# Performance work log

Measured on AMD Instinct MI355X. Metric: run time of the kernel, lower is better.

## Reference

```python
import jax, jax.numpy as jnp
import numpy as np

B, H, S, D = 4, 8, 2048, 64

def setup_inputs() -> dict:
    key = jax.random.key(0)
    k1, k2 = jax.random.split(key)
    q = jax.random.normal(k1, (B, H, S, D), dtype=jnp.float32)
    kv = jax.random.normal(k2, (B, H, S, D), dtype=jnp.float32)
    mask = jnp.zeros((1, 1, S, S), dtype=jnp.float32)
    return {"q": q, "kv": kv, "mask": mask}

def reference(q, kv, mask):
    # score = q @ kv^T / sqrt(d_k) + mask ; softmax over last dim ; @ kv
    d_k = jnp.asarray(kv.shape[-1], dtype=q.dtype)
    score = jnp.einsum('bhqd,bhkd->bhqk', q, kv) / jnp.sqrt(d_k)
    score = score + mask
    attn = jax.nn.softmax(score, axis=-1)
    out = jnp.einsum('bhqk,bhkd->bhqd', attn, kv)
    return out
```

## Files before the change

kernel.cpp:

```cpp
#include <hip/hip_runtime.h>
#include <hip/hip_bf16.h>
#include <stdint.h>


typedef __bf16 bf16;
typedef __attribute__((ext_vector_type(8))) __bf16 bf16x8;
typedef __attribute__((ext_vector_type(4))) __bf16 bf16x4;
typedef __attribute__((ext_vector_type(4))) float floatx4;
typedef __attribute__((ext_vector_type(16))) float floatx16;
typedef __attribute__((ext_vector_type(4))) int int4v;
typedef __attribute__((ext_vector_type(2))) unsigned int uint2v;

#define SLEN 2048
#define DH   64
#define BR   64
#define BC   64
#define NKT  (SLEN / BC)
#define NQT  (SLEN / BR)
#define BH_N 32
#define LOG2E 1.44269504088896341f

#define IMGE_G 4096

#define AS1 __attribute__((address_space(1)))
#define AS3 __attribute__((address_space(3)))

static __device__ inline float fexp2(float x) {
    return __builtin_amdgcn_exp2f(x);
}

static_assert(BH_N == NQT, "prep kernel folds bh and qt onto one grid axis");

__global__ __launch_bounds__(256) void kv_prep(
    const float* __restrict__ kv, const float* __restrict__ mask,
    bf16* __restrict__ kvK, bf16* __restrict__ kvT, int* __restrict__ flags)
{
    __shared__ bf16 Tl[64 * 72];
    __shared__ int wany[4];
    const int kt = blockIdx.x, z = blockIdx.y;
    const int t = threadIdx.x;

    float acc = 0.f;
#pragma unroll
    for (int i = 0; i < 4; ++i) {
        int f = i * 256 + t;
        int row = f >> 4, c4 = (f & 15) * 4;
        const float4 v = *(const float4*)(mask + (size_t)(z * BR + row) * SLEN + kt * BC + c4);
        acc = fmaxf(acc, fmaxf(fmaxf(fabsf(v.x), fabsf(v.y)), fmaxf(fabsf(v.z), fabsf(v.w))));
    }
    unsigned long long any = __ballot(acc != 0.f);
    if ((t & 63) == 0) wany[t >> 6] = (any != 0ull) ? 1 : 0;

    const float* src = kv + ((size_t)z * SLEN + kt * BC) * DH;
#pragma unroll
    for (int i = 0; i < 4; ++i) {
        int f = i * 256 + t;
        int key = f >> 4, d4 = (f & 15) * 4;
        float4 v = *(const float4*)(src + (size_t)key * DH + d4);
        bf16x4 b; b[0] = (bf16)v.x; b[1] = (bf16)v.y; b[2] = (bf16)v.z; b[3] = (bf16)v.w;
        *(bf16x4*)&Tl[key * 72 + d4] = b;
    }
    __syncthreads();
    if (t == 0) flags[z * NKT + kt] = wany[0] | wany[1] | wany[2] | wany[3];

    bf16* outK = kvK + ((size_t)z * NKT + kt) * IMGE_G;
#pragma unroll
    for (int i = 0; i < 2; ++i) {
        int G = i * 256 + t;
        int u = G >> 8, ss = (G >> 6) & 3, ln = G & 63;
        int key = u * 32 + (ln & 31), d0 = 16 * ss + 8 * (ln >> 5);
        bf16x8 w = *(const bf16x8*)&Tl[key * 72 + d0];
        *(bf16x8*)(outK + (size_t)G * 8) = w;
    }
    bf16* outV = kvT + ((size_t)z * NKT + kt) * IMGE_G;
#pragma unroll
    for (int i = 0; i < 2; ++i) {
        int G = i * 256 + t;
        int dt = G >> 8, u = (G >> 7) & 1, ff = (G >> 6) & 1, ln = G & 63;
        int d = dt * 32 + (ln & 31), kb = u * 32 + 16 * ff + 8 * (ln >> 5);
        bf16x8 w;
#pragma unroll
        for (int j = 0; j < 8; ++j)
            w[j] = Tl[(kb + j) * 72 + d];
        *(bf16x8*)(outV + (size_t)G * 8) = w;
    }
}

__global__ __launch_bounds__(256) void attn_fwd20(
    const float* __restrict__ q, const float* __restrict__ mask,
    const int* __restrict__ flags,
    const bf16* __restrict__ kvK, const bf16* __restrict__ kvT,
    float* __restrict__ out)
{
    __shared__ __align__(16) float Obuf[2 * 2 * 4 * 64 * 4];
    __shared__ float Lbuf[2 * 64];

    const int bh = blockIdx.x;
    const int qt = blockIdx.y;
    const int q0 = qt * 64;
    const int t = threadIdx.x;
    const int w = t >> 6, lane = t & 63;
    const int qg = w & 1, kh = w >> 1;
    const int r5 = lane & 31, h = lane >> 5;

    const float qscale = 0.125f * LOG2E;
    bf16x8 qf[4];
    {
        const float* qrow = q + ((size_t)bh * SLEN + q0 + qg * 32 + r5) * DH;
#pragma unroll
        for (int s = 0; s < 4; ++s) {
            float4 f0 = *(const float4*)(qrow + 16 * s + 8 * h);
            float4 f1 = *(const float4*)(qrow + 16 * s + 8 * h + 4);
            bf16x8 a;
            a[0] = (bf16)(f0.x * qscale); a[1] = (bf16)(f0.y * qscale);
            a[2] = (bf16)(f0.z * qscale); a[3] = (bf16)(f0.w * qscale);
            a[4] = (bf16)(f1.x * qscale); a[5] = (bf16)(f1.y * qscale);
            a[6] = (bf16)(f1.z * qscale); a[7] = (bf16)(f1.w * qscale);
            qf[s] = a;
        }
    }

    unsigned fmask;
    {
        int ld = (lane < 32) ? flags[qt * NKT + lane] : 0;
        fmask = (unsigned)__ballot(ld != 0);
    }

    floatx16 o[2];
#pragma unroll
    for (int dt = 0; dt < 2; ++dt)
#pragma unroll
        for (int i = 0; i < 16; ++i) o[dt][i] = 0.f;
    float l_run = 0.f;

    const char* Kb = (const char*)(kvK + (size_t)bh * NKT * IMGE_G) + lane * 16;
    const char* Vb = (const char*)(kvT + (size_t)bh * NKT * IMGE_G) + lane * 16;

    bf16x8 ka0, ka1, ka2, ka3, va0, va1, va2, va3;
    bf16x8 kb0, kb1, kb2, kb3, vb0, vb1, vb2, vb3;

#define LOAD_SUB(K0,K1,K2,K3,V0,V1,V2,V3, j)                                  \
    {                                                                          \
        const int jj = (j) & 31;                                               \
        const char* Kt = Kb + (size_t)(kh * 16 + (jj >> 1)) * 8192 + (jj & 1) * 4096; \
        const char* Vt = Vb + (size_t)(kh * 16 + (jj >> 1)) * 8192 + (jj & 1) * 2048; \
        K0 = *(const bf16x8*)(Kt);                                             \
        K1 = *(const bf16x8*)(Kt + 1024);                                      \
        K2 = *(const bf16x8*)(Kt + 2048);                                      \
        K3 = *(const bf16x8*)(Kt + 3072);                                      \
        V0 = *(const bf16x8*)(Vt);                                             \
        V1 = *(const bf16x8*)(Vt + 1024);                                      \
        V2 = *(const bf16x8*)(Vt + 4096);                                      \
        V3 = *(const bf16x8*)(Vt + 4096 + 1024);                               \
    }

#define COMPUTE_SUB(K0,K1,K2,K3,V0,V1,V2,V3, j)                               \
    {                                                                          \
        const int jj = (j);                                                    \
        const int kt_ = kh * 16 + (jj >> 1);                                   \
        floatx16 s;                                                            \
        _Pragma("unroll")                                                      \
        for (int i = 0; i < 16; ++i) s[i] = 0.f;                               \
        s = __builtin_amdgcn_mfma_f32_32x32x16_bf16(K0, qf[0], s, 0, 0, 0);    \
        s = __builtin_amdgcn_mfma_f32_32x32x16_bf16(K1, qf[1], s, 0, 0, 0);    \
        s = __builtin_amdgcn_mfma_f32_32x32x16_bf16(K2, qf[2], s, 0, 0, 0);    \
        s = __builtin_amdgcn_mfma_f32_32x32x16_bf16(K3, qf[3], s, 0, 0, 0);    \
        if ((fmask >> kt_) & 1u) {                                             \
            const float* mrow = mask + (size_t)(q0 + qg * 32 + r5) * SLEN      \
                                + kt_ * 64 + (jj & 1) * 32 + 4 * h;            \
            _Pragma("unroll")                                                  \
            for (int g4 = 0; g4 < 4; ++g4) {                                   \
                float4 mv = *(const float4*)(mrow + 8 * g4);                   \
                s[4 * g4 + 0] += mv.x * LOG2E;                                 \
                s[4 * g4 + 1] += mv.y * LOG2E;                                 \
                s[4 * g4 + 2] += mv.z * LOG2E;                                 \
                s[4 * g4 + 3] += mv.w * LOG2E;                                 \
            }                                                                  \
        }                                                                      \
        _Pragma("unroll")                                                      \
        for (int i = 0; i < 16; ++i) s[i] = fexp2(s[i]);                       \
        l_run += ((s[0] + s[1]) + (s[2] + s[3]))                               \
               + ((s[4] + s[5]) + (s[6] + s[7]))                               \
               + ((s[8] + s[9]) + (s[10] + s[11]))                             \
               + ((s[12] + s[13]) + (s[14] + s[15]));                          \
        bf16x4 lA = { (bf16)s[0],  (bf16)s[1],  (bf16)s[2],  (bf16)s[3]  };    \
        bf16x4 hA = { (bf16)s[4],  (bf16)s[5],  (bf16)s[6],  (bf16)s[7]  };    \
        bf16x4 lB = { (bf16)s[8],  (bf16)s[9],  (bf16)s[10], (bf16)s[11] };    \
        bf16x4 hB = { (bf16)s[12], (bf16)s[13], (bf16)s[14], (bf16)s[15] };    \
        uint2v xA = __builtin_bit_cast(uint2v, lA);                            \
        uint2v yA = __builtin_bit_cast(uint2v, hA);                            \
        uint2v xB = __builtin_bit_cast(uint2v, lB);                            \
        uint2v yB = __builtin_bit_cast(uint2v, hB);                            \
        uint2v sA0 = __builtin_amdgcn_permlane32_swap(xA[0], yA[0], false, false); \
        uint2v sA1 = __builtin_amdgcn_permlane32_swap(xA[1], yA[1], false, false); \
        uint2v sB0 = __builtin_amdgcn_permlane32_swap(xB[0], yB[0], false, false); \
        uint2v sB1 = __builtin_amdgcn_permlane32_swap(xB[1], yB[1], false, false); \
        int4v pAi = { (int)sA0[0], (int)sA1[0], (int)sA0[1], (int)sA1[1] };    \
        int4v pBi = { (int)sB0[0], (int)sB1[0], (int)sB0[1], (int)sB1[1] };    \
        bf16x8 pfA = __builtin_bit_cast(bf16x8, pAi);                          \
        bf16x8 pfB = __builtin_bit_cast(bf16x8, pBi);                          \
        o[0] = __builtin_amdgcn_mfma_f32_32x32x16_bf16(V0, pfA, o[0], 0, 0, 0); \
        o[0] = __builtin_amdgcn_mfma_f32_32x32x16_bf16(V1, pfB, o[0], 0, 0, 0); \
        o[1] = __builtin_amdgcn_mfma_f32_32x32x16_bf16(V2, pfA, o[1], 0, 0, 0); \
        o[1] = __builtin_amdgcn_mfma_f32_32x32x16_bf16(V3, pfB, o[1], 0, 0, 0); \
    }

    LOAD_SUB(ka0, ka1, ka2, ka3, va0, va1, va2, va3, 0)

    for (int it = 0; it < 16; ++it) {
        const int j0 = 2 * it, j1 = 2 * it + 1;
        LOAD_SUB(kb0, kb1, kb2, kb3, vb0, vb1, vb2, vb3, j1)
        COMPUTE_SUB(ka0, ka1, ka2, ka3, va0, va1, va2, va3, j0)
        LOAD_SUB(ka0, ka1, ka2, ka3, va0, va1, va2, va3, j1 + 1)
        COMPUTE_SUB(kb0, kb1, kb2, kb3, vb0, vb1, vb2, vb3, j1)
    }
#undef LOAD_SUB
#undef COMPUTE_SUB

    __syncthreads();
    if (kh == 1) {
#pragma unroll
        for (int dt = 0; dt < 2; ++dt)
#pragma unroll
            for (int k = 0; k < 4; ++k) {
                float4 v;
                v.x = o[dt][4 * k + 0]; v.y = o[dt][4 * k + 1];
                v.z = o[dt][4 * k + 2]; v.w = o[dt][4 * k + 3];
                *(float4*)(Obuf + ((size_t)((qg * 2 + dt) * 4 + k) * 64 + lane) * 4) = v;
            }
        Lbuf[qg * 64 + lane] = l_run;
    }
    __syncthreads();
    if (kh == 0) {
        float lsum = l_run + Lbuf[qg * 64 + lane];
        float l = lsum + __shfl_xor(lsum, 32);
        float inv = 1.f / l;
        float* ob = out + ((size_t)bh * SLEN + q0 + qg * 32 + r5) * DH + 4 * h;
#pragma unroll
        for (int dt = 0; dt < 2; ++dt)
#pragma unroll
            for (int k = 0; k < 4; ++k) {
                float4 p = *(const float4*)(Obuf + ((size_t)((qg * 2 + dt) * 4 + k) * 64 + lane) * 4);
                float4 v;
                v.x = (o[dt][4 * k + 0] + p.x) * inv;
                v.y = (o[dt][4 * k + 1] + p.y) * inv;
                v.z = (o[dt][4 * k + 2] + p.z) * inv;
                v.w = (o[dt][4 * k + 3] + p.w) * inv;
                *(float4*)(ob + dt * 32 + 8 * k) = v;
            }
    }
}

#define LDT 72
__global__ __launch_bounds__(256) void attn_mask_flags(
    const float* __restrict__ mask, int* __restrict__ flags)
{
    const int kt = blockIdx.x, qt = blockIdx.y;
    const int t = threadIdx.x;
    float acc = 0.f;
#pragma unroll
    for (int i = 0; i < 4; ++i) {
        int f = i * 256 + t;
        int row = f >> 4, c4 = (f & 15) * 4;
        const float4 v = *(const float4*)(mask + (size_t)(qt * BR + row) * SLEN + kt * BC + c4);
        acc = fmaxf(acc, fmaxf(fmaxf(fabsf(v.x), fabsf(v.y)), fmaxf(fabsf(v.z), fabsf(v.w))));
    }
    unsigned long long any = __ballot(acc != 0.f);
    __shared__ int wany[4];
    if ((t & 63) == 0) wany[t >> 6] = (any != 0ull) ? 1 : 0;
    __syncthreads();
    if (t == 0) flags[qt * NKT + kt] = wany[0] | wany[1] | wany[2] | wany[3];
}

__global__ __launch_bounds__(256) void attn_fwd(
    const float* __restrict__ q, const float* __restrict__ kv,
    const float* __restrict__ mask, const int* __restrict__ flags,
    float* __restrict__ out)
{
    __shared__ __align__(16) bf16 Kl[BC * LDT];
    __shared__ __align__(16) bf16 Vt[DH * LDT];
    __shared__ __align__(16) bf16 Pl[BR * LDT];

    const int qt = blockIdx.x;
    const int bh = blockIdx.y;
    const int q0 = qt * BR;
    const int t = threadIdx.x;
    const int wave = t >> 6, lane = t & 63;
    const int ln16 = lane & 15, quad = lane >> 4;

    const float qscale = 0.125f * LOG2E;
    bf16x8 aq[2];
    {
        const float* qrow = q + ((size_t)bh * SLEN + q0 + wave * 16 + ln16) * DH;
#pragma unroll
        for (int kc = 0; kc < 2; ++kc) {
            float4 f0 = *(const float4*)(qrow + kc * 32 + quad * 8);
            float4 f1 = *(const float4*)(qrow + kc * 32 + quad * 8 + 4);
            bf16x8 a;
            a[0] = (bf16)(f0.x * qscale); a[1] = (bf16)(f0.y * qscale);
            a[2] = (bf16)(f0.z * qscale); a[3] = (bf16)(f0.w * qscale);
            a[4] = (bf16)(f1.x * qscale); a[5] = (bf16)(f1.y * qscale);
            a[6] = (bf16)(f1.z * qscale); a[7] = (bf16)(f1.w * qscale);
            aq[kc] = a;
        }
    }

    floatx4 o[4];
#pragma unroll
    for (int dt = 0; dt < 4; ++dt) o[dt] = (floatx4){0.f, 0.f, 0.f, 0.f};
    float m_run[4], l_run[4];
#pragma unroll
    for (int r = 0; r < 4; ++r) { m_run[r] = -3.0e38f; l_run[r] = 0.f; }

    const float* kvb = kv + (size_t)bh * SLEN * DH;

    for (int kt = 0; kt < NKT; ++kt) {
        float4 st[4];
        const float* kvt = kvb + (size_t)kt * BC * DH;
#pragma unroll
        for (int i = 0; i < 4; ++i) {
            int f = i * 256 + t;
            st[i] = *(const float4*)(kvt + (size_t)f * 4);
        }
        __syncthreads();
#pragma unroll
        for (int i = 0; i < 4; ++i) {
            int f = i * 256 + t;
            int key = f >> 4, d4 = (f & 15) * 4;
            bf16 b0 = (bf16)st[i].x, b1 = (bf16)st[i].y, b2 = (bf16)st[i].z, b3 = (bf16)st[i].w;
            *(bf16x4*)&Kl[key * LDT + d4] = (bf16x4){b0, b1, b2, b3};
            Vt[(d4 + 0) * LDT + key] = b0;
            Vt[(d4 + 1) * LDT + key] = b1;
            Vt[(d4 + 2) * LDT + key] = b2;
            Vt[(d4 + 3) * LDT + key] = b3;
        }
        __syncthreads();

        floatx4 s[4];
#pragma unroll
        for (int nt = 0; nt < 4; ++nt) {
            s[nt] = (floatx4){0.f, 0.f, 0.f, 0.f};
#pragma unroll
            for (int kc = 0; kc < 2; ++kc) {
                bf16x8 bk = *(const bf16x8*)&Kl[(ln16 + 16 * nt) * LDT + kc * 32 + quad * 8];
                s[nt] = __builtin_amdgcn_mfma_f32_16x16x32_bf16(aq[kc], bk, s[nt], 0, 0, 0);
            }
        }

        if (!flags || flags[qt * NKT + kt]) {
            const float* mrow = mask + (size_t)(q0 + quad * 4) * SLEN + kt * BC + ln16;
#pragma unroll
            for (int r = 0; r < 4; ++r)
#pragma unroll
                for (int nt = 0; nt < 4; ++nt)
                    s[nt][r] += mrow[(size_t)r * SLEN + nt * 16] * LOG2E;
        }

#pragma unroll
        for (int r = 0; r < 4; ++r) {
            float mx = fmaxf(fmaxf(s[0][r], s[1][r]), fmaxf(s[2][r], s[3][r]));
            mx = fmaxf(mx, __shfl_xor(mx, 1));
            mx = fmaxf(mx, __shfl_xor(mx, 2));
            mx = fmaxf(mx, __shfl_xor(mx, 4));
            mx = fmaxf(mx, __shfl_xor(mx, 8));
            float mnew = fmaxf(m_run[r], mx);
            float alpha = exp2f(m_run[r] - mnew);
            m_run[r] = mnew;
            float rs = 0.f;
#pragma unroll
            for (int nt = 0; nt < 4; ++nt) {
                float p = exp2f(s[nt][r] - mnew);
                s[nt][r] = p;
                rs += p;
            }
            rs += __shfl_xor(rs, 1);
            rs += __shfl_xor(rs, 2);
            rs += __shfl_xor(rs, 4);
            rs += __shfl_xor(rs, 8);
            l_run[r] = l_run[r] * alpha + rs;
#pragma unroll
            for (int dt = 0; dt < 4; ++dt) o[dt][r] *= alpha;
        }

#pragma unroll
        for (int nt = 0; nt < 4; ++nt)
#pragma unroll
            for (int r = 0; r < 4; ++r)
                Pl[(wave * 16 + quad * 4 + r) * LDT + ln16 + 16 * nt] = (bf16)s[nt][r];

#pragma unroll
        for (int kc2 = 0; kc2 < 2; ++kc2) {
            bf16x8 pfr = *(const bf16x8*)&Pl[(wave * 16 + ln16) * LDT + kc2 * 32 + quad * 8];
#pragma unroll
            for (int dt = 0; dt < 4; ++dt) {
                bf16x8 vfr = *(const bf16x8*)&Vt[(ln16 + 16 * dt) * LDT + kc2 * 32 + quad * 8];
                o[dt] = __builtin_amdgcn_mfma_f32_16x16x32_bf16(pfr, vfr, o[dt], 0, 0, 0);
            }
        }
    }

#pragma unroll
    for (int r = 0; r < 4; ++r) {
        float inv = 1.0f / l_run[r];
        int qrow = q0 + wave * 16 + quad * 4 + r;
        float* orow = out + ((size_t)bh * SLEN + qrow) * DH;
#pragma unroll
        for (int dt = 0; dt < 4; ++dt)
            orow[ln16 + 16 * dt] = o[dt][r] * inv;
    }
}

extern "C" void kernel_launch(void* const* d_in, const int* in_sizes, int n_in,
                              void* d_out, int out_size, void* d_ws, size_t ws_size,
                              hipStream_t stream)
{
    const float* q    = (const float*)d_in[0];
    const float* kv   = (const float*)d_in[1];
    const float* mask = (const float*)d_in[2];
    float* out = (float*)d_out;

    const size_t kvKoff = 4096;
    const size_t kvToff = kvKoff + (size_t)BH_N * NKT * IMGE_G * 2;
    const size_t need   = kvToff + (size_t)BH_N * NKT * IMGE_G * 2;

    if (ws_size >= need) {
        int*  flags = (int*)d_ws;
        bf16* kvK   = (bf16*)((char*)d_ws + kvKoff);
        bf16* kvT   = (bf16*)((char*)d_ws + kvToff);
        kv_prep<<<dim3(NKT, BH_N), 256, 0, stream>>>(kv, mask, kvK, kvT, flags);
        attn_fwd20<<<dim3(BH_N, SLEN / 64), 256, 0, stream>>>(q, mask, flags, kvK, kvT, out);
    } else {
        int* flags = nullptr;
        if (ws_size >= (size_t)NQT * NKT * sizeof(int)) {
            flags = (int*)d_ws;
            attn_mask_flags<<<dim3(NKT, NQT), 256, 0, stream>>>(mask, flags);
        }
        attn_fwd<<<dim3(NQT, BH_N), 256, 0, stream>>>(q, kv, mask, flags, out);
    }
}
```

Before: 139.4 us.

## Use 512-thread blocks over 128 query rows and software-pipeline QK with softmax/PV

Each block now covers 128 query rows with 8 waves (4 query groups by 2 key halves) instead of 64 rows with 4 waves, so blocks sharing a bh reuse the same K/V stream across more queries. The inner loop is restructured so the QK MFMAs for the next sub-tile are issued before the exp/PV work of the current one. V loads move into the finish step, so only K is double-buffered in registers. The aim is to overlap matrix work with exponentials and cut register pressure, at the risk of fewer blocks (512 instead of 1024) and exposed V load latency.

```diff
diff --git a/kernel.cpp b/kernel.cpp
--- a/kernel.cpp
+++ b/kernel.cpp
@@ -86,21 +86,21 @@
     }
 }
 
-__global__ __launch_bounds__(256) void attn_fwd20(
+__global__ __launch_bounds__(512) void attn_fwd25(
     const float* __restrict__ q, const float* __restrict__ mask,
     const int* __restrict__ flags,
     const bf16* __restrict__ kvK, const bf16* __restrict__ kvT,
     float* __restrict__ out)
 {
-    __shared__ __align__(16) float Obuf[2 * 2 * 4 * 64 * 4];
-    __shared__ float Lbuf[2 * 64];
+    __shared__ __align__(16) float Obuf[4 * 2 * 4 * 64 * 4];
+    __shared__ float Lbuf[4 * 64];
 
     const int bh = blockIdx.x;
     const int qt = blockIdx.y;
-    const int q0 = qt * 64;
+    const int q0 = qt * 128;
     const int t = threadIdx.x;
     const int w = t >> 6, lane = t & 63;
-    const int qg = w & 1, kh = w >> 1;
+    const int qg = w & 3, kh = w >> 2;
     const int r5 = lane & 31, h = lane >> 5;
 
     const float qscale = 0.125f * LOG2E;
@@ -120,114 +120,121 @@
         }
     }
 
+    const int fqt = qt * 2 + (qg >> 1);
     unsigned fmask;
     {
-        int ld = (lane < 32) ? flags[qt * NKT + lane] : 0;
+        int ld = (lane < 32) ? flags[fqt * NKT + lane] : 0;
         fmask = (unsigned)__ballot(ld != 0);
     }
 
-    floatx16 o[2];
-#pragma unroll
-    for (int dt = 0; dt < 2; ++dt)
-#pragma unroll
-        for (int i = 0; i < 16; ++i) o[dt][i] = 0.f;
+    floatx16 o0, o1;
+#pragma unroll
+    for (int i = 0; i < 16; ++i) { o0[i] = 0.f; o1[i] = 0.f; }
     float l_run = 0.f;
 
     const char* Kb = (const char*)(kvK + (size_t)bh * NKT * IMGE_G) + lane * 16;
     const char* Vb = (const char*)(kvT + (size_t)bh * NKT * IMGE_G) + lane * 16;
 
-    bf16x8 ka0, ka1, ka2, ka3, va0, va1, va2, va3;
-    bf16x8 kb0, kb1, kb2, kb3, vb0, vb1, vb2, vb3;
-
-#define LOAD_SUB(K0,K1,K2,K3,V0,V1,V2,V3, j)                                  \
+    bf16x8 kA0, kA1, kA2, kA3, kB0, kB1, kB2, kB3;
+    floatx16 sA, sB;
+
+#define LOADK(K0,K1,K2,K3, j)                                                  \
     {                                                                          \
-        const int jj = (j) & 31;                                               \
-        const char* Kt = Kb + (size_t)(kh * 16 + (jj >> 1)) * 8192 + (jj & 1) * 4096; \
-        const char* Vt = Vb + (size_t)(kh * 16 + (jj >> 1)) * 8192 + (jj & 1) * 2048; \
-        K0 = *(const bf16x8*)(Kt);                                             \
-        K1 = *(const bf16x8*)(Kt + 1024);                                      \
-        K2 = *(const bf16x8*)(Kt + 2048);                                      \
-        K3 = *(const bf16x8*)(Kt + 3072);                                      \
-        V0 = *(const bf16x8*)(Vt);                                             \
-        V1 = *(const bf16x8*)(Vt + 1024);                                      \
-        V2 = *(const bf16x8*)(Vt + 4096);                                      \
-        V3 = *(const bf16x8*)(Vt + 4096 + 1024);                               \
-    }
-
-#define COMPUTE_SUB(K0,K1,K2,K3,V0,V1,V2,V3, j)                               \
+        const char* Kt_ = Kb + (size_t)(kh * 16 + (((j) & 31) >> 1)) * 8192    \
+                          + ((j) & 1) * 4096;                                  \
+        K0 = *(const bf16x8*)(Kt_);                                            \
+        K1 = *(const bf16x8*)(Kt_ + 1024);                                     \
+        K2 = *(const bf16x8*)(Kt_ + 2048);                                     \
+        K3 = *(const bf16x8*)(Kt_ + 3072);                                     \
+    }
+
+#define QK(S, K0,K1,K2,K3)                                                     \
     {                                                                          \
-        const int jj = (j);                                                    \
-        const int kt_ = kh * 16 + (jj >> 1);                                   \
-        floatx16 s;                                                            \
         _Pragma("unroll")                                                      \
-        for (int i = 0; i < 16; ++i) s[i] = 0.f;                               \
-        s = __builtin_amdgcn_mfma_f32_32x32x16_bf16(K0, qf[0], s, 0, 0, 0);    \
-        s = __builtin_amdgcn_mfma_f32_32x32x16_bf16(K1, qf[1], s, 0, 0, 0);    \
-        s = __builtin_amdgcn_mfma_f32_32x32x16_bf16(K2, qf[2], s, 0, 0, 0);    \
-        s = __builtin_amdgcn_mfma_f32_32x32x16_bf16(K3, qf[3], s, 0, 0, 0);    \
+        for (int i = 0; i < 16; ++i) S[i] = 0.f;                               \
+        S = __builtin_amdgcn_mfma_f32_32x32x16_bf16(K0, qf[0], S, 0, 0, 0);    \
+        S = __builtin_amdgcn_mfma_f32_32x32x16_bf16(K1, qf[1], S, 0, 0, 0);    \
+        S = __builtin_amdgcn_mfma_f32_32x32x16_bf16(K2, qf[2], S, 0, 0, 0);    \
+        S = __builtin_amdgcn_mfma_f32_32x32x16_bf16(K3, qf[3], S, 0, 0, 0);    \
+    }
+
+#define FINISH(S, j)                                                           \
+    {                                                                          \
+        const int kt_ = kh * 16 + ((j) >> 1);                                  \
+        const char* Vt_ = Vb + (size_t)kt_ * 8192 + ((j) & 1) * 2048;          \
+        bf16x8 v00 = *(const bf16x8*)(Vt_);                                    \
+        bf16x8 v01 = *(const bf16x8*)(Vt_ + 1024);                             \
+        bf16x8 v10 = *(const bf16x8*)(Vt_ + 4096);                             \
+        bf16x8 v11 = *(const bf16x8*)(Vt_ + 4096 + 1024);                      \
         if ((fmask >> kt_) & 1u) {                                             \
             const float* mrow = mask + (size_t)(q0 + qg * 32 + r5) * SLEN      \
-                                + kt_ * 64 + (jj & 1) * 32 + 4 * h;            \
+                                + kt_ * 64 + ((j) & 1) * 32 + 4 * h;           \
             _Pragma("unroll")                                                  \
             for (int g4 = 0; g4 < 4; ++g4) {                                   \
                 float4 mv = *(const float4*)(mrow + 8 * g4);                   \
-                s[4 * g4 + 0] += mv.x * LOG2E;                                 \
-                s[4 * g4 + 1] += mv.y * LOG2E;                                 \
-                s[4 * g4 + 2] += mv.z * LOG2E;                                 \
-                s[4 * g4 + 3] += mv.w * LOG2E;                                 \
+                S[4 * g4 + 0] += mv.x * LOG2E;                                 \
+                S[4 * g4 + 1] += mv.y * LOG2E;                                 \
+                S[4 * g4 + 2] += mv.z * LOG2E;                                 \
+                S[4 * g4 + 3] += mv.w * LOG2E;                                 \
             }                                                                  \
         }                                                                      \
         _Pragma("unroll")                                                      \
-        for (int i = 0; i < 16; ++i) s[i] = fexp2(s[i]);                       \
-        l_run += ((s[0] + s[1]) + (s[2] + s[3]))                               \
-               + ((s[4] + s[5]) + (s[6] + s[7]))                               \
-               + ((s[8] + s[9]) + (s[10] + s[11]))                             \
-               + ((s[12] + s[13]) + (s[14] + s[15]));                          \
-        bf16x4 lA = { (bf16)s[0],  (bf16)s[1],  (bf16)s[2],  (bf16)s[3]  };    \
-        bf16x4 hA = { (bf16)s[4],  (bf16)s[5],  (bf16)s[6],  (bf16)s[7]  };    \
-        bf16x4 lB = { (bf16)s[8],  (bf16)s[9],  (bf16)s[10], (bf16)s[11] };    \
-        bf16x4 hB = { (bf16)s[12], (bf16)s[13], (bf16)s[14], (bf16)s[15] };    \
+        for (int i = 0; i < 16; ++i) S[i] = fexp2(S[i]);                       \
+        l_run += ((S[0] + S[1]) + (S[2] + S[3]))                               \
+               + ((S[4] + S[5]) + (S[6] + S[7]))                               \
+               + ((S[8] + S[9]) + (S[10] + S[11]))                             \
+               + ((S[12] + S[13]) + (S[14] + S[15]));                          \
+        bf16x4 lA = { (bf16)S[0],  (bf16)S[1],  (bf16)S[2],  (bf16)S[3]  };    \
+        bf16x4 hA = { (bf16)S[4],  (bf16)S[5],  (bf16)S[6],  (bf16)S[7]  };    \
+        bf16x4 lB = { (bf16)S[8],  (bf16)S[9],  (bf16)S[10], (bf16)S[11] };    \
+        bf16x4 hB = { (bf16)S[12], (bf16)S[13], (bf16)S[14], (bf16)S[15] };    \
         uint2v xA = __builtin_bit_cast(uint2v, lA);                            \
         uint2v yA = __builtin_bit_cast(uint2v, hA);                            \
         uint2v xB = __builtin_bit_cast(uint2v, lB);                            \
         uint2v yB = __builtin_bit_cast(uint2v, hB);                            \
-        uint2v sA0 = __builtin_amdgcn_permlane32_swap(xA[0], yA[0], false, false); \
-        uint2v sA1 = __builtin_amdgcn_permlane32_swap(xA[1], yA[1], false, false); \
-        uint2v sB0 = __builtin_amdgcn_permlane32_swap(xB[0], yB[0], false, false); \
-        uint2v sB1 = __builtin_amdgcn_permlane32_swap(xB[1], yB[1], false, false); \
-        int4v pAi = { (int)sA0[0], (int)sA1[0], (int)sA0[1], (int)sA1[1] };    \
-        int4v pBi = { (int)sB0[0], (int)sB1[0], (int)sB0[1], (int)sB1[1] };    \
+        uint2v sw0 = __builtin_amdgcn_permlane32_swap(xA[0], yA[0], false, false); \
+        uint2v sw1 = __builtin_amdgcn_permlane32_swap(xA[1], yA[1], false, false); \
+        uint2v sw2 = __builtin_amdgcn_permlane32_swap(xB[0], yB[0], false, false); \
+        uint2v sw3 = __builtin_amdgcn_permlane32_swap(xB[1], yB[1], false, false); \
+        int4v pAi = { (int)sw0[0], (int)sw1[0], (int)sw0[1], (int)sw1[1] };    \
+        int4v pBi = { (int)sw2[0], (int)sw3[0], (int)sw2[1], (int)sw3[1] };    \
         bf16x8 pfA = __builtin_bit_cast(bf16x8, pAi);                          \
         bf16x8 pfB = __builtin_bit_cast(bf16x8, pBi);                          \
-        o[0] = __builtin_amdgcn_mfma_f32_32x32x16_bf16(V0, pfA, o[0], 0, 0, 0); \
-        o[0] = __builtin_amdgcn_mfma_f32_32x32x16_bf16(V1, pfB, o[0], 0, 0, 0); \
-        o[1] = __builtin_amdgcn_mfma_f32_32x32x16_bf16(V2, pfA, o[1], 0, 0, 0); \
-        o[1] = __builtin_amdgcn_mfma_f32_32x32x16_bf16(V3, pfB, o[1], 0, 0, 0); \
-    }
-
-    LOAD_SUB(ka0, ka1, ka2, ka3, va0, va1, va2, va3, 0)
+        o0 = __builtin_amdgcn_mfma_f32_32x32x16_bf16(v00, pfA, o0, 0, 0, 0);   \
+        o1 = __builtin_amdgcn_mfma_f32_32x32x16_bf16(v10, pfA, o1, 0, 0, 0);   \
+        o0 = __builtin_amdgcn_mfma_f32_32x32x16_bf16(v01, pfB, o0, 0, 0, 0);   \
+        o1 = __builtin_amdgcn_mfma_f32_32x32x16_bf16(v11, pfB, o1, 0, 0, 0);   \
+    }
+
+    LOADK(kA0, kA1, kA2, kA3, 0)
+    QK(sA, kA0, kA1, kA2, kA3)
 
     for (int it = 0; it < 16; ++it) {
         const int j0 = 2 * it, j1 = 2 * it + 1;
-        LOAD_SUB(kb0, kb1, kb2, kb3, vb0, vb1, vb2, vb3, j1)
-        COMPUTE_SUB(ka0, ka1, ka2, ka3, va0, va1, va2, va3, j0)
-        LOAD_SUB(ka0, ka1, ka2, ka3, va0, va1, va2, va3, j1 + 1)
-        COMPUTE_SUB(kb0, kb1, kb2, kb3, vb0, vb1, vb2, vb3, j1)
-    }
-#undef LOAD_SUB
-#undef COMPUTE_SUB
+        LOADK(kB0, kB1, kB2, kB3, j1)
+        FINISH(sA, j0)
+        QK(sB, kB0, kB1, kB2, kB3)
+        LOADK(kA0, kA1, kA2, kA3, j1 + 1)
+        FINISH(sB, j1)
+        QK(sA, kA0, kA1, kA2, kA3)
+    }
+#undef LOADK
+#undef QK
+#undef FINISH
 
     __syncthreads();
     if (kh == 1) {
 #pragma unroll
-        for (int dt = 0; dt < 2; ++dt)
+        for (int dt = 0; dt < 2; ++dt) {
+            const floatx16& oo = dt ? o1 : o0;
 #pragma unroll
             for (int k = 0; k < 4; ++k) {
                 float4 v;
-                v.x = o[dt][4 * k + 0]; v.y = o[dt][4 * k + 1];
-                v.z = o[dt][4 * k + 2]; v.w = o[dt][4 * k + 3];
+                v.x = oo[4 * k + 0]; v.y = oo[4 * k + 1];
+                v.z = oo[4 * k + 2]; v.w = oo[4 * k + 3];
                 *(float4*)(Obuf + ((size_t)((qg * 2 + dt) * 4 + k) * 64 + lane) * 4) = v;
             }
+        }
         Lbuf[qg * 64 + lane] = l_run;
     }
     __syncthreads();
@@ -237,17 +244,19 @@
         float inv = 1.f / l;
         float* ob = out + ((size_t)bh * SLEN + q0 + qg * 32 + r5) * DH + 4 * h;
 #pragma unroll
-        for (int dt = 0; dt < 2; ++dt)
+        for (int dt = 0; dt < 2; ++dt) {
+            const floatx16& oo = dt ? o1 : o0;
 #pragma unroll
             for (int k = 0; k < 4; ++k) {
                 float4 p = *(const float4*)(Obuf + ((size_t)((qg * 2 + dt) * 4 + k) * 64 + lane) * 4);
                 float4 v;
-                v.x = (o[dt][4 * k + 0] + p.x) * inv;
-                v.y = (o[dt][4 * k + 1] + p.y) * inv;
-                v.z = (o[dt][4 * k + 2] + p.z) * inv;
-                v.w = (o[dt][4 * k + 3] + p.w) * inv;
+                v.x = (oo[4 * k + 0] + p.x) * inv;
+                v.y = (oo[4 * k + 1] + p.y) * inv;
+                v.z = (oo[4 * k + 2] + p.z) * inv;
+                v.w = (oo[4 * k + 3] + p.w) * inv;
                 *(float4*)(ob + dt * 32 + 8 * k) = v;
             }
+        }
     }
 }
 
@@ -428,7 +437,7 @@
         bf16* kvK   = (bf16*)((char*)d_ws + kvKoff);
         bf16* kvT   = (bf16*)((char*)d_ws + kvToff);
         kv_prep<<<dim3(NKT, BH_N), 256, 0, stream>>>(kv, mask, kvK, kvT, flags);
-        attn_fwd20<<<dim3(BH_N, SLEN / 64), 256, 0, stream>>>(q, mask, flags, kvK, kvT, out);
+        attn_fwd25<<<dim3(BH_N, SLEN / 128), 512, 0, stream>>>(q, mask, flags, kvK, kvT, out);
     } else {
         int* flags = nullptr;
         if (ws_size >= (size_t)NQT * NKT * sizeof(int)) {
```

New measurement: 136.6 us. 1.02x faster.
